# Kernel optimization log

Hardware: AMD Instinct MI355X
Metric: run time of the kernel (lower is better)

Reference implementation:

```python
import jax, jax.numpy as jnp
import numpy as np

H = 1024      # hidden_size
V = 32000     # output_size (vocab)
L = 512       # max_length (encoder positions)
B = 256       # batch


def setup_inputs() -> dict:
    key = jax.random.key(0)
    ks = jax.random.split(key, 12)
    s = 0.02
    return {
        "input": jax.random.randint(ks[0], (B,), 0, V),
        "hidden": jax.random.normal(ks[1], (1, B, H), jnp.float32),
        "encoder_outputs": jax.random.normal(ks[2], (L, H), jnp.float32),
        # learned params (PyTorch layout: Linear weight is [out, in])
        "emb": jax.random.normal(ks[3], (V, H), jnp.float32) * s,
        "attn_W": jax.random.normal(ks[4], (L, 2 * H), jnp.float32) * s,
        "attn_b": jnp.zeros((L,), jnp.float32),
        "comb_W": jax.random.normal(ks[5], (H, 2 * H), jnp.float32) * s,
        "comb_b": jnp.zeros((H,), jnp.float32),
        "W_ih": jax.random.normal(ks[6], (3 * H, H), jnp.float32) * s,
        "W_hh": jax.random.normal(ks[7], (3 * H, H), jnp.float32) * s,
        "b_ih": jnp.zeros((3 * H,), jnp.float32),
        "b_hh": jnp.zeros((3 * H,), jnp.float32),
        "out_W": jax.random.normal(ks[8], (V, H), jnp.float32) * s,
        "out_b": jnp.zeros((V,), jnp.float32),
    }


def reference(input, hidden, encoder_outputs, emb, attn_W, attn_b,
              comb_W, comb_b, W_ih, W_hh, b_ih, b_hh, out_W, out_b):
    h = hidden[0]                                   # [B,H]
    embedded = emb[input]                           # [B,H] (dropout in eval mode = identity)
    attn_logits = jnp.concatenate([embedded, h], axis=1) @ attn_W.T + attn_b
    attn_weights = jax.nn.softmax(attn_logits, axis=1)        # [B,L]
    attn_applied = attn_weights @ encoder_outputs              # [B,H]
    x = jnp.concatenate([embedded, attn_applied], axis=1) @ comb_W.T + comb_b
    x = jax.nn.relu(x)                                         # [B,H]
    # single-step GRU (PyTorch gate layout: r, z, n)
    gi = x @ W_ih.T + b_ih                                     # [B,3H]
    gh = h @ W_hh.T + b_hh                                     # [B,3H]
    gi_r, gi_z, gi_n = jnp.split(gi, 3, axis=1)
    gh_r, gh_z, gh_n = jnp.split(gh, 3, axis=1)
    r = jax.nn.sigmoid(gi_r + gh_r)
    z = jax.nn.sigmoid(gi_z + gh_z)
    n = jnp.tanh(gi_n + r * gh_n)
    h_new = (1.0 - z) * n + z * h                              # [B,H]
    output = jax.nn.log_softmax(h_new @ out_W.T + out_b, axis=1)  # [B,V]
    return output, h_new[None], attn_weights
```

## Files before the change

### kernel.cpp

```cpp
#include <hip/hip_runtime.h>
#include <hip/hip_bf16.h>
#include <cstdint>

#define DEVI __device__ __forceinline__

typedef __bf16 bf16x8 __attribute__((ext_vector_type(8)));
typedef float  f32x4  __attribute__((ext_vector_type(4)));

constexpr int Hdim = 1024;
constexpr int Vdim = 32000;
constexpr int Ldim = 512;
constexpr int Bdim = 256;

DEVI unsigned short f2bf(float f) {
  __bf16 h = (__bf16)f;
  return __builtin_bit_cast(unsigned short, h);
}

DEVI void load_lds16(const void* g, void* l) {
  __builtin_amdgcn_global_load_lds(
      (const __attribute__((address_space(1))) unsigned int*)g,
      (__attribute__((address_space(3))) unsigned int*)l, 16, 0, 0);
}

constexpr int GF_NKT = 32;

__global__ __launch_bounds__(256, 2)
void gemm_flat(const unsigned short* __restrict__ A,
               const float* __restrict__ W,
               const float* __restrict__ bias,
               float* __restrict__ C,
               float2* __restrict__ plse)
{
  __shared__ float lW[4][64 * 32];

  const int t    = threadIdx.x;
  const int lane = t & 63;
  const int wv   = t >> 6;
  const int r16  = lane & 15;
  const int k8   = (lane >> 4) * 8;
  const int s0   = (lane >> 4) * 2;
  const int n0   = blockIdx.x * 64;
  const int drow0 = wv * 16 + (lane >> 3);

  uint4 aset[4][4];
  f32x4 acc[4][4];
#pragma unroll
  for (int m = 0; m < 4; ++m)
#pragma unroll
    for (int n = 0; n < 4; ++n)
#pragma unroll
      for (int r = 0; r < 4; ++r) acc[m][n][r] = 0.f;

#define ISSUE_A(SET, KT) do {                                                  \
    const int ko_ = (KT) * 32 + k8;                                            \
    _Pragma("unroll")                                                          \
    for (int m = 0; m < 4; ++m)                                                \
      aset[SET][m] = *reinterpret_cast<const uint4*>(                          \
          A + (size_t)(wv * 64 + m * 16 + r16) * 1024 + ko_);                  \
  } while (0)

#define ISSUE_W(BUF, KT) do {                                                  \
    _Pragma("unroll")                                                          \
    for (int q = 0; q < 2; ++q) {                                              \
      const int row_ = drow0 + q * 8;                                          \
      const float* src_ = W + (size_t)(n0 + row_) * 1024 + (KT) * 32           \
                          + (((lane & 7) ^ (row_ & 7)) * 4);                   \
      load_lds16(src_, &lW[BUF][(wv * 2 + q) * 256]);                          \
    }                                                                          \
  } while (0)

#define STEP_COMPUTE(P) do {                                                   \
    bf16x8 bw[4];                                                              \
    _Pragma("unroll")                                                          \
    for (int n = 0; n < 4; ++n) {                                              \
      const int row_ = n * 16 + r16;                                           \
      const int sw_  = row_ & 7;                                               \
      f32x4 w0 = *reinterpret_cast<const f32x4*>(                              \
          &lW[P][row_ * 32 + ((s0 ^ sw_) * 4)]);                               \
      f32x4 w1 = *reinterpret_cast<const f32x4*>(                              \
          &lW[P][row_ * 32 + (((s0 + 1) ^ sw_) * 4)]);                         \
      bf16x8 v;                                                                \
      v[0] = (__bf16)w0[0]; v[1] = (__bf16)w0[1];                              \
      v[2] = (__bf16)w0[2]; v[3] = (__bf16)w0[3];                              \
      v[4] = (__bf16)w1[0]; v[5] = (__bf16)w1[1];                              \
      v[6] = (__bf16)w1[2]; v[7] = (__bf16)w1[3];                              \
      bw[n] = v;                                                               \
    }                                                                          \
    _Pragma("unroll")                                                          \
    for (int m = 0; m < 4; ++m) {                                              \
      bf16x8 am = __builtin_bit_cast(bf16x8, aset[P][m]);                      \
      _Pragma("unroll")                                                        \
      for (int n = 0; n < 4; ++n)                                              \
        acc[m][n] = __builtin_amdgcn_mfma_f32_16x16x32_bf16(am, bw[n],         \
                                                            acc[m][n], 0,0,0);\
    }                                                                          \
  } while (0)

#define STEP(P, I) do {                                                        \
    asm volatile("s_waitcnt vmcnt(12)" ::: "memory");                          \
    __builtin_amdgcn_sched_barrier(0);                                         \
    __builtin_amdgcn_s_barrier();                                              \
    __builtin_amdgcn_sched_barrier(0);                                         \
    { const int kn_ = ((I) + 3 < GF_NKT) ? (I) + 3 : GF_NKT - 1;               \
      ISSUE_A((P + 3) & 3, kn_); ISSUE_W((P + 3) & 3, kn_); }                  \
    __builtin_amdgcn_sched_barrier(0);                                         \
    STEP_COMPUTE(P);                                                           \
    __builtin_amdgcn_sched_barrier(0);                                         \
  } while (0)

  ISSUE_A(0, 0); ISSUE_W(0, 0);
  ISSUE_A(1, 1); ISSUE_W(1, 1);
  ISSUE_A(2, 2); ISSUE_W(2, 2);

  for (int ib = 0; ib < GF_NKT; ib += 4) {
    STEP(0, ib);
    STEP(1, ib + 1);
    STEP(2, ib + 2);
    STEP(3, ib + 3);
  }

#undef STEP
#undef STEP_COMPUTE
#undef ISSUE_W
#undef ISSUE_A

#pragma unroll
  for (int n = 0; n < 4; ++n) {
    const int col = n0 + n * 16 + r16;
    const float bv = bias[col];
#pragma unroll
    for (int m = 0; m < 4; ++m) {
      const int rbase = wv * 64 + m * 16 + (lane >> 4) * 4;
#pragma unroll
      for (int r = 0; r < 4; ++r) {
        const float v = acc[m][n][r] + bv;
        acc[m][n][r] = v;
        C[(size_t)(rbase + r) * Vdim + col] = v;
      }
    }
  }
#pragma unroll
  for (int m = 0; m < 4; ++m) {
#pragma unroll
    for (int r = 0; r < 4; ++r) {
      float mx = fmaxf(fmaxf(acc[m][0][r], acc[m][1][r]),
                       fmaxf(acc[m][2][r], acc[m][3][r]));
#pragma unroll
      for (int o = 1; o < 16; o <<= 1) mx = fmaxf(mx, __shfl_xor(mx, o, 16));
      float s = 0.f;
#pragma unroll
      for (int n = 0; n < 4; ++n) s += __expf(acc[m][n][r] - mx);
#pragma unroll
      for (int o = 1; o < 16; o <<= 1) s += __shfl_xor(s, o, 16);
      if (r16 == 0) {
        const int row = wv * 64 + m * 16 + (lane >> 4) * 4 + r;
        plse[(size_t)row * gridDim.x + blockIdx.x] = make_float2(mx, s);
      }
    }
  }
}

template<int WM, bool ABF16, bool DUAL>
__global__ __launch_bounds__(256, 2)
void gemm_bt(const void* __restrict__ Av0, const float* __restrict__ Wt0,
             const void* __restrict__ Av1, const float* __restrict__ Wt1,
             const float* __restrict__ bias,
             float* __restrict__ C0, float* __restrict__ C1,
             int K, int ldc, int col_off, int act, int aact0,
             int nsplit)
{
  constexpr int MT    = 4 * WM;
  constexpr int PITCH = 40;
  constexpr int ITA   = MT / 32;
  constexpr int MR    = WM / 16;

  __shared__ unsigned short lA[2 * MT * PITCH];
  __shared__ unsigned short lW[2 * 64 * PITCH];

  const int t  = threadIdx.x;
  const int m0 = blockIdx.y * MT;
  const int n0 = blockIdx.x * 64;

  int kz = blockIdx.z, half = 0;
  if (DUAL) { half = (kz >= nsplit) ? 1 : 0; kz -= half * nsplit; }
  const int NK = K / (32 * nsplit);
  const int kb = kz * NK;

  const void*  Av = (DUAL && half) ? Av1 : Av0;
  const float* Wt = (DUAL && half) ? Wt1 : Wt0;
  float*       C  = (DUAL && half) ? C1  : C0;
  const int  aact = (DUAL && half) ? 0 : aact0;

  const int tr = t >> 3;
  const int tc = (t & 7) * 4;

  const float*          Af = ABF16 ? nullptr : ((const float*)Av) + (size_t)m0 * K;
  const unsigned short* Ab = ABF16 ? ((const unsigned short*)Av) + (size_t)m0 * K : nullptr;
  const float*          Wb = Wt + (size_t)n0 * K;

  const int lane = t & 63;
  const int wv   = t >> 6;
  const int r16  = lane & 15;
  const int k8   = (lane >> 4) * 8;

  f32x4 acc[MR][4];
#pragma unroll
  for (int m = 0; m < MR; ++m)
#pragma unroll
    for (int n = 0; n < 4; ++n)
#pragma unroll
      for (int r = 0; r < 4; ++r) acc[m][n][r] = 0.f;

  struct RS { f32x4 ra[ITA]; ushort4 rab[ITA]; f32x4 rw[2]; };

  auto loadT = [&](RS& rg, int kt) {
    const int ko = (kb + kt) * 32 + tc;
    if constexpr (ABF16) {
      const unsigned short* ap = Ab + ko;
#pragma unroll
      for (int i = 0; i < ITA; ++i)
        rg.rab[i] = *reinterpret_cast<const ushort4*>(ap + (size_t)(tr + 32 * i) * K);
    } else {
      const float* ap = Af + ko;
#pragma unroll
      for (int i = 0; i < ITA; ++i)
        rg.ra[i] = *reinterpret_cast<const f32x4*>(ap + (size_t)(tr + 32 * i) * K);
    }
    const float* wp = Wb + ko;
#pragma unroll
    for (int i = 0; i < 2; ++i)
      rg.rw[i] = *reinterpret_cast<const f32x4*>(wp + (size_t)(tr + 32 * i) * K);
  };

  auto storeT = [&](RS& rg, int bo) {
    unsigned short* sA = &lA[bo * MT * PITCH];
    unsigned short* sW = &lW[bo * 64 * PITCH];
#pragma unroll
    for (int i = 0; i < ITA; ++i) {
      ushort4 u;
      if constexpr (ABF16) u = rg.rab[i];
      else {
        f32x4 v = rg.ra[i];
        if (aact) { v[0]=fmaxf(v[0],0.f); v[1]=fmaxf(v[1],0.f);
                    v[2]=fmaxf(v[2],0.f); v[3]=fmaxf(v[3],0.f); }
        u.x = f2bf(v[0]); u.y = f2bf(v[1]); u.z = f2bf(v[2]); u.w = f2bf(v[3]);
      }
      *reinterpret_cast<ushort4*>(&sA[(tr + 32 * i) * PITCH + tc]) = u;
    }
#pragma unroll
    for (int i = 0; i < 2; ++i) {
      f32x4 v = rg.rw[i]; ushort4 u;
      u.x = f2bf(v[0]); u.y = f2bf(v[1]); u.z = f2bf(v[2]); u.w = f2bf(v[3]);
      *reinterpret_cast<ushort4*>(&sW[(tr + 32 * i) * PITCH + tc]) = u;
    }
  };

  auto comp = [&](int bo) {
    const unsigned short* sA = &lA[bo * MT * PITCH];
    const unsigned short* sW = &lW[bo * 64 * PITCH];
    bf16x8 af[MR], bfr[4];
#pragma unroll
    for (int m = 0; m < MR; ++m)
      af[m] = *reinterpret_cast<const bf16x8*>(&sA[(wv * WM + m * 16 + r16) * PITCH + k8]);
#pragma unroll
    for (int n = 0; n < 4; ++n)
      bfr[n] = *reinterpret_cast<const bf16x8*>(&sW[(n * 16 + r16) * PITCH + k8]);
#pragma unroll
    for (int m = 0; m < MR; ++m)
#pragma unroll
      for (int n = 0; n < 4; ++n)
        acc[m][n] = __builtin_amdgcn_mfma_f32_16x16x32_bf16(af[m], bfr[n], acc[m][n], 0, 0, 0);
  };

#define GB_BARRIER() do { \
    asm volatile("s_waitcnt lgkmcnt(0)" ::: "memory"); \
    __builtin_amdgcn_sched_barrier(0); \
    __builtin_amdgcn_s_barrier(); \
  } while (0)

  RS ra_, rb_;
  loadT(ra_, 0);
  loadT(rb_, 1);
  storeT(ra_, 0);
  GB_BARRIER();

  for (int kt = 0; kt < NK; kt += 2) {
    if (kt + 2 < NK) loadT(ra_, kt + 2);
    comp(0);
    storeT(rb_, 1);
    GB_BARRIER();
    if (kt + 3 < NK) loadT(rb_, kt + 3);
    comp(1);
    if (kt + 2 < NK) {
      storeT(ra_, 0);
      GB_BARRIER();
    }
  }
#undef GB_BARRIER

#pragma unroll
  for (int n = 0; n < 4; ++n) {
    const int col = n0 + n * 16 + r16;
    const float bv = (bias && nsplit == 1) ? bias[col] : 0.f;
#pragma unroll
    for (int m = 0; m < MR; ++m) {
      const int rbase = m0 + wv * WM + m * 16 + (lane >> 4) * 4;
#pragma unroll
      for (int r = 0; r < 4; ++r) {
        float v = acc[m][n][r] + bv;
        if (act) v = fmaxf(v, 0.f);
        if (nsplit > 1) {
          atomicAdd(&C[(size_t)(rbase + r) * ldc + col_off + col], v);
        } else {
          C[(size_t)(rbase + r) * ldc + col_off + col] = v;
        }
      }
    }
  }
}

__global__ void prep_kernel(const int* __restrict__ ids, const float* __restrict__ hid,
                            const float* __restrict__ emb,
                            const float* __restrict__ attn_b, const float* __restrict__ comb_b,
                            const float* __restrict__ b_ih, const float* __restrict__ b_hh,
                            float* __restrict__ X0, float* __restrict__ X1,
                            float* __restrict__ alog, float* __restrict__ xact,
                            float* __restrict__ gi, float* __restrict__ gh)
{
  const int b = blockIdx.x, t = threadIdx.x;
  const int row = ids[b];
  f32x4 e = *reinterpret_cast<const f32x4*>(emb + (size_t)row * Hdim + t * 4);
  *reinterpret_cast<f32x4*>(X0 + (size_t)b * 2048 + t * 4) = e;
  *reinterpret_cast<f32x4*>(X1 + (size_t)b * 2048 + t * 4) = e;
  f32x4 h = *reinterpret_cast<const f32x4*>(hid + (size_t)b * Hdim + t * 4);
  *reinterpret_cast<f32x4*>(X0 + (size_t)b * 2048 + 1024 + t * 4) = h;
  f32x4 z4 = {0.f, 0.f, 0.f, 0.f};
  *reinterpret_cast<f32x4*>(X1 + (size_t)b * 2048 + 1024 + t * 4) = z4;
  if (t < 128)
    *reinterpret_cast<f32x4*>(alog + (size_t)b * Ldim + t * 4) =
        *reinterpret_cast<const f32x4*>(attn_b + t * 4);
  *reinterpret_cast<f32x4*>(xact + (size_t)b * Hdim + t * 4) =
      *reinterpret_cast<const f32x4*>(comb_b + t * 4);
#pragma unroll
  for (int i = 0; i < 3; ++i) {
    *reinterpret_cast<f32x4*>(gi + (size_t)b * 3072 + i * 1024 + t * 4) =
        *reinterpret_cast<const f32x4*>(b_ih + i * 1024 + t * 4);
    *reinterpret_cast<f32x4*>(gh + (size_t)b * 3072 + i * 1024 + t * 4) =
        *reinterpret_cast<const f32x4*>(b_hh + i * 1024 + t * 4);
  }
}

__global__ void transpose_kernel(const float* __restrict__ enc, float* __restrict__ encT)
{
  __shared__ float tile[64][65];
  const int l0 = blockIdx.x * 64, h0 = blockIdx.y * 64;
  const int t = threadIdx.x;
  const int c = t & 63, rr = t >> 6;
#pragma unroll
  for (int p = 0; p < 16; ++p) {
    const int r = p * 4 + rr;
    tile[r][c] = enc[(size_t)(l0 + r) * Hdim + h0 + c];
  }
  __syncthreads();
#pragma unroll
  for (int p = 0; p < 16; ++p) {
    const int r = p * 4 + rr;
    encT[(size_t)(h0 + r) * Ldim + l0 + c] = tile[c][r];
  }
}

__global__ void attn_softmax_kernel(const float* __restrict__ logits, float* __restrict__ wout)
{
  __shared__ float red[256];
  const int b = blockIdx.x, t = threadIdx.x;
  const float x0 = logits[b * Ldim + t];
  const float x1 = logits[b * Ldim + 256 + t];
  red[t] = fmaxf(x0, x1); __syncthreads();
  for (int o = 128; o > 0; o >>= 1) { if (t < o) red[t] = fmaxf(red[t], red[t + o]); __syncthreads(); }
  const float m = red[0]; __syncthreads();
  const float e0 = __expf(x0 - m), e1 = __expf(x1 - m);
  red[t] = e0 + e1; __syncthreads();
  for (int o = 128; o > 0; o >>= 1) { if (t < o) red[t] += red[t + o]; __syncthreads(); }
  const float inv = 1.f / red[0];
  wout[b * Ldim + t]       = e0 * inv;
  wout[b * Ldim + 256 + t] = e1 * inv;
}

DEVI float sigm(float x) { return 1.f / (1.f + __expf(-x)); }

__global__ void gru_kernel(const float* __restrict__ gi, const float* __restrict__ gh,
                           const float* __restrict__ hin,
                           float* __restrict__ hnew, unsigned short* __restrict__ hnbf)
{
  const int idx = blockIdx.x * 256 + threadIdx.x;
  const int b = idx >> 10, j = idx & 1023;
  const float* gib = gi + (size_t)b * 3072;
  const float* ghb = gh + (size_t)b * 3072;
  const float r = sigm(gib[j] + ghb[j]);
  const float z = sigm(gib[1024 + j] + ghb[1024 + j]);
  const float n = tanhf(gib[2048 + j] + r * ghb[2048 + j]);
  const float h = hin[idx];
  const float hn = (1.f - z) * n + z * h;
  hnew[idx] = hn;
  hnbf[idx] = f2bf(hn);
}

__global__ void lse_reduce(const float2* __restrict__ part, int npart,
                           float* __restrict__ lse)
{
  __shared__ float rm[256], rs[256];
  const int b = blockIdx.x, t = threadIdx.x;
  float m = -1e30f, s = 0.f;
  for (int j = t; j < npart; j += 256) {
    const float2 p = part[(size_t)b * npart + j];
    const float nm = fmaxf(m, p.x);
    s = s * __expf(m - nm) + p.y * __expf(p.x - nm);
    m = nm;
  }
  rm[t] = m; rs[t] = s; __syncthreads();
  for (int o = 128; o > 0; o >>= 1) {
    if (t < o) {
      const float m2 = rm[t + o], s2 = rs[t + o];
      const float nm = fmaxf(rm[t], m2);
      rs[t] = rs[t] * __expf(rm[t] - nm) + s2 * __expf(m2 - nm);
      rm[t] = nm;
    }
    __syncthreads();
  }
  if (t == 0) lse[b] = rm[0] + __logf(rs[0]);
}

__global__ void lsm_sub(const float* __restrict__ lse, float* __restrict__ out)
{
  const int b = blockIdx.x >> 3, c = blockIdx.x & 7;
  const float l = lse[b];
  f32x4* row4 = reinterpret_cast<f32x4*>(out + (size_t)b * Vdim) + c * 1000;
  for (int i = threadIdx.x; i < 1000; i += 256) {
    f32x4 x = row4[i];
    x[0] -= l; x[1] -= l; x[2] -= l; x[3] -= l;
    row4[i] = x;
  }
}

extern "C" void kernel_launch(void* const* d_in, const int* in_sizes, int n_in,
                              void* d_out, int out_size, void* d_ws, size_t ws_size,
                              hipStream_t stream)
{
  (void)in_sizes; (void)n_in; (void)out_size; (void)ws_size;

  const int*   ids    = (const int*)  d_in[0];
  const float* hid    = (const float*)d_in[1];
  const float* enc    = (const float*)d_in[2];
  const float* emb    = (const float*)d_in[3];
  const float* attn_W = (const float*)d_in[4];
  const float* attn_b = (const float*)d_in[5];
  const float* comb_W = (const float*)d_in[6];
  const float* comb_b = (const float*)d_in[7];
  const float* W_ih   = (const float*)d_in[8];
  const float* W_hh   = (const float*)d_in[9];
  const float* b_ih   = (const float*)d_in[10];
  const float* b_hh   = (const float*)d_in[11];
  const float* out_W  = (const float*)d_in[12];
  const float* out_b  = (const float*)d_in[13];

  float* out_logits = (float*)d_out;
  float* out_h      = out_logits + (size_t)Bdim * Vdim;
  float* out_attw   = out_h + (size_t)Bdim * Hdim;

  char* w = (char*)d_ws;
  float* X0   = (float*)w; w += (size_t)Bdim * 2048 * 4;
  float* X1   = (float*)w; w += (size_t)Bdim * 2048 * 4;
  float* encT = (float*)w; w += (size_t)Hdim * Ldim * 4;
  float* alog = (float*)w; w += (size_t)Bdim * Ldim * 4;
  float* xact = (float*)w; w += (size_t)Bdim * Hdim * 4;
  float* gi   = (float*)w; w += (size_t)Bdim * 3 * Hdim * 4;
  float* gh   = (float*)w; w += (size_t)Bdim * 3 * Hdim * 4;
  unsigned short* hnbf = (unsigned short*)w; w += (size_t)Bdim * Hdim * 2;
  float2* plse = (float2*)w; w += (size_t)Bdim * (Vdim / 64) * 8;
  float* lse  = (float*)w; w += (size_t)Bdim * 4;

  prep_kernel<<<Bdim, 256, 0, stream>>>(ids, hid, emb, attn_b, comb_b, b_ih, b_hh,
                                        X0, X1, alog, xact, gi, gh);
  transpose_kernel<<<dim3(Ldim / 64, Hdim / 64), 256, 0, stream>>>(enc, encT);

  gemm_bt<32, false, false><<<dim3(Ldim / 64, 2, 8), 256, 0, stream>>>(
      X0, attn_W, nullptr, nullptr, nullptr, alog, nullptr,
      2048, Ldim, 0, 0, 0, 8);
  attn_softmax_kernel<<<Bdim, 256, 0, stream>>>(alog, out_attw);

  gemm_bt<32, false, false><<<dim3(Hdim / 64, 2, 4), 256, 0, stream>>>(
      out_attw, encT, nullptr, nullptr, nullptr, X1, nullptr,
      512, 2048, 1024, 0, 0, 4);

  gemm_bt<32, false, false><<<dim3(Hdim / 64, 2, 8), 256, 0, stream>>>(
      X1, comb_W, nullptr, nullptr, nullptr, xact, nullptr,
      2048, Hdim, 0, 0, 0, 8);

  gemm_bt<32, false, true><<<dim3(3 * Hdim / 64, 2, 8), 256, 0, stream>>>(
      xact, W_ih, hid, W_hh, nullptr, gi, gh,
      1024, 3 * Hdim, 0, 0, 1, 4);

  gru_kernel<<<Bdim * Hdim / 256, 256, 0, stream>>>(gi, gh, hid, out_h, hnbf);

  gemm_flat<<<Vdim / 64, 256, 0, stream>>>(hnbf, out_W, out_b, out_logits, plse);

  lse_reduce<<<Bdim, 256, 0, stream>>>(plse, Vdim / 64, lse);
  lsm_sub<<<Bdim * 8, 256, 0, stream>>>(lse, out_logits);
}
```

Measured before the change: 138.0 us.

## Stage full-K bf16 weight tile in LDS for output projection GEMM

Replaces the pipelined output-projection GEMM with a variant where each block handles 32 vocab columns, converts the whole 32x1024 weight slice to bf16 once into swizzled LDS, and then streams A with simple double-buffered register prefetch. This drops the per-step fp32-to-bf16 conversion, the LDS round trips of fp32 weights and the per-step barriers. In exchange it doubles the grid and the partial logsumexp entries, uses 64KB of LDS per block, which limits occupancy, and reloads A from global memory for every block.

```diff
diff --git a/kernel.cpp b/kernel.cpp
--- a/kernel.cpp
+++ b/kernel.cpp
@@ -17,116 +17,87 @@
   return __builtin_bit_cast(unsigned short, h);
 }
 
-DEVI void load_lds16(const void* g, void* l) {
-  __builtin_amdgcn_global_load_lds(
-      (const __attribute__((address_space(1))) unsigned int*)g,
-      (__attribute__((address_space(3))) unsigned int*)l, 16, 0, 0);
-}
-
-constexpr int GF_NKT = 32;
-
 __global__ __launch_bounds__(256, 2)
-void gemm_flat(const unsigned short* __restrict__ A,
-               const float* __restrict__ W,
-               const float* __restrict__ bias,
-               float* __restrict__ C,
-               float2* __restrict__ plse)
-{
-  __shared__ float lW[4][64 * 32];
+void gemm_flat2(const unsigned short* __restrict__ A,
+                const float* __restrict__ W,
+                const float* __restrict__ bias,
+                float* __restrict__ C,
+                float2* __restrict__ plse)
+{
+  __shared__ unsigned short lW[32 * 1024];
 
   const int t    = threadIdx.x;
   const int lane = t & 63;
   const int wv   = t >> 6;
   const int r16  = lane & 15;
   const int k8   = (lane >> 4) * 8;
-  const int s0   = (lane >> 4) * 2;
-  const int n0   = blockIdx.x * 64;
-  const int drow0 = wv * 16 + (lane >> 3);
-
-  uint4 aset[4][4];
-  f32x4 acc[4][4];
+  const int n0   = blockIdx.x * 32;
+
+  f32x4 acc[4][2];
 #pragma unroll
   for (int m = 0; m < 4; ++m)
 #pragma unroll
-    for (int n = 0; n < 4; ++n)
+    for (int n = 0; n < 2; ++n)
 #pragma unroll
       for (int r = 0; r < 4; ++r) acc[m][n][r] = 0.f;
 
-#define ISSUE_A(SET, KT) do {                                                  \
+#pragma unroll 2
+  for (int r = 0; r < 8; ++r) {
+    const int row = wv * 8 + r;
+    const float* src = W + (size_t)(n0 + row) * 1024;
+    f32x4 v[4];
+#pragma unroll
+    for (int j = 0; j < 4; ++j)
+      v[j] = *reinterpret_cast<const f32x4*>(src + j * 256 + lane * 4);
+#pragma unroll
+    for (int j = 0; j < 4; ++j) {
+      ushort4 u;
+      u.x = f2bf(v[j][0]); u.y = f2bf(v[j][1]);
+      u.z = f2bf(v[j][2]); u.w = f2bf(v[j][3]);
+      const int byte = row * 2048 + (j * 64 + lane) * 8;
+      *reinterpret_cast<ushort4*>((char*)lW + (byte ^ ((row & 7) << 4))) = u;
+    }
+  }
+
+  uint4 apf0[4], apf1[4];
+
+#define LOADA(ARR, KT) do {                                                    \
     const int ko_ = (KT) * 32 + k8;                                            \
     _Pragma("unroll")                                                          \
     for (int m = 0; m < 4; ++m)                                                \
-      aset[SET][m] = *reinterpret_cast<const uint4*>(                          \
+      ARR[m] = *reinterpret_cast<const uint4*>(                                \
           A + (size_t)(wv * 64 + m * 16 + r16) * 1024 + ko_);                  \
   } while (0)
 
-#define ISSUE_W(BUF, KT) do {                                                  \
+#define COMP(ARR, KT) do {                                                     \
     _Pragma("unroll")                                                          \
-    for (int q = 0; q < 2; ++q) {                                              \
-      const int row_ = drow0 + q * 8;                                          \
-      const float* src_ = W + (size_t)(n0 + row_) * 1024 + (KT) * 32           \
-                          + (((lane & 7) ^ (row_ & 7)) * 4);                   \
-      load_lds16(src_, &lW[BUF][(wv * 2 + q) * 256]);                          \
+    for (int n = 0; n < 2; ++n) {                                              \
+      const int nr_  = n * 16 + r16;                                           \
+      const int rby_ = nr_ * 2048 + (KT) * 64 + (lane >> 4) * 16;              \
+      bf16x8 bw = *reinterpret_cast<const bf16x8*>(                            \
+          (const char*)lW + (rby_ ^ ((nr_ & 7) << 4)));                        \
+      _Pragma("unroll")                                                        \
+      for (int m = 0; m < 4; ++m)                                              \
+        acc[m][n] = __builtin_amdgcn_mfma_f32_16x16x32_bf16(                   \
+            __builtin_bit_cast(bf16x8, ARR[m]), bw, acc[m][n], 0, 0, 0);       \
     }                                                                          \
   } while (0)
 
-#define STEP_COMPUTE(P) do {                                                   \
-    bf16x8 bw[4];                                                              \
-    _Pragma("unroll")                                                          \
-    for (int n = 0; n < 4; ++n) {                                              \
-      const int row_ = n * 16 + r16;                                           \
-      const int sw_  = row_ & 7;                                               \
-      f32x4 w0 = *reinterpret_cast<const f32x4*>(                              \
-          &lW[P][row_ * 32 + ((s0 ^ sw_) * 4)]);                               \
-      f32x4 w1 = *reinterpret_cast<const f32x4*>(                              \
-          &lW[P][row_ * 32 + (((s0 + 1) ^ sw_) * 4)]);                         \
-      bf16x8 v;                                                                \
-      v[0] = (__bf16)w0[0]; v[1] = (__bf16)w0[1];                              \
-      v[2] = (__bf16)w0[2]; v[3] = (__bf16)w0[3];                              \
-      v[4] = (__bf16)w1[0]; v[5] = (__bf16)w1[1];                              \
-      v[6] = (__bf16)w1[2]; v[7] = (__bf16)w1[3];                              \
-      bw[n] = v;                                                               \
-    }                                                                          \
-    _Pragma("unroll")                                                          \
-    for (int m = 0; m < 4; ++m) {                                              \
-      bf16x8 am = __builtin_bit_cast(bf16x8, aset[P][m]);                      \
-      _Pragma("unroll")                                                        \
-      for (int n = 0; n < 4; ++n)                                              \
-        acc[m][n] = __builtin_amdgcn_mfma_f32_16x16x32_bf16(am, bw[n],         \
-                                                            acc[m][n], 0,0,0);\
-    }                                                                          \
-  } while (0)
-
-#define STEP(P, I) do {                                                        \
-    asm volatile("s_waitcnt vmcnt(12)" ::: "memory");                          \
-    __builtin_amdgcn_sched_barrier(0);                                         \
-    __builtin_amdgcn_s_barrier();                                              \
-    __builtin_amdgcn_sched_barrier(0);                                         \
-    { const int kn_ = ((I) + 3 < GF_NKT) ? (I) + 3 : GF_NKT - 1;               \
-      ISSUE_A((P + 3) & 3, kn_); ISSUE_W((P + 3) & 3, kn_); }                  \
-    __builtin_amdgcn_sched_barrier(0);                                         \
-    STEP_COMPUTE(P);                                                           \
-    __builtin_amdgcn_sched_barrier(0);                                         \
-  } while (0)
-
-  ISSUE_A(0, 0); ISSUE_W(0, 0);
-  ISSUE_A(1, 1); ISSUE_W(1, 1);
-  ISSUE_A(2, 2); ISSUE_W(2, 2);
-
-  for (int ib = 0; ib < GF_NKT; ib += 4) {
-    STEP(0, ib);
-    STEP(1, ib + 1);
-    STEP(2, ib + 2);
-    STEP(3, ib + 3);
-  }
-
-#undef STEP
-#undef STEP_COMPUTE
-#undef ISSUE_W
-#undef ISSUE_A
-
-#pragma unroll
-  for (int n = 0; n < 4; ++n) {
+  LOADA(apf0, 0);
+  __syncthreads();
+
+  for (int kt = 0; kt < 32; kt += 2) {
+    LOADA(apf1, kt + 1);
+    COMP(apf0, kt);
+    LOADA(apf0, (kt + 2 < 32) ? kt + 2 : 31);
+    COMP(apf1, kt + 1);
+  }
+
+#undef COMP
+#undef LOADA
+
+#pragma unroll
+  for (int n = 0; n < 2; ++n) {
     const int col = n0 + n * 16 + r16;
     const float bv = bias[col];
 #pragma unroll
@@ -144,13 +115,10 @@
   for (int m = 0; m < 4; ++m) {
 #pragma unroll
     for (int r = 0; r < 4; ++r) {
-      float mx = fmaxf(fmaxf(acc[m][0][r], acc[m][1][r]),
-                       fmaxf(acc[m][2][r], acc[m][3][r]));
+      float mx = fmaxf(acc[m][0][r], acc[m][1][r]);
 #pragma unroll
       for (int o = 1; o < 16; o <<= 1) mx = fmaxf(mx, __shfl_xor(mx, o, 16));
-      float s = 0.f;
-#pragma unroll
-      for (int n = 0; n < 4; ++n) s += __expf(acc[m][n][r] - mx);
+      float s = __expf(acc[m][0][r] - mx) + __expf(acc[m][1][r] - mx);
 #pragma unroll
       for (int o = 1; o < 16; o <<= 1) s += __shfl_xor(s, o, 16);
       if (r16 == 0) {
@@ -477,7 +445,7 @@
   float* gi   = (float*)w; w += (size_t)Bdim * 3 * Hdim * 4;
   float* gh   = (float*)w; w += (size_t)Bdim * 3 * Hdim * 4;
   unsigned short* hnbf = (unsigned short*)w; w += (size_t)Bdim * Hdim * 2;
-  float2* plse = (float2*)w; w += (size_t)Bdim * (Vdim / 64) * 8;
+  float2* plse = (float2*)w; w += (size_t)Bdim * (Vdim / 32) * 8;
   float* lse  = (float*)w; w += (size_t)Bdim * 4;
 
   prep_kernel<<<Bdim, 256, 0, stream>>>(ids, hid, emb, attn_b, comb_b, b_ih, b_hh,
@@ -503,8 +471,8 @@
 
   gru_kernel<<<Bdim * Hdim / 256, 256, 0, stream>>>(gi, gh, hid, out_h, hnbf);
 
-  gemm_flat<<<Vdim / 64, 256, 0, stream>>>(hnbf, out_W, out_b, out_logits, plse);
-
-  lse_reduce<<<Bdim, 256, 0, stream>>>(plse, Vdim / 64, lse);
+  gemm_flat2<<<Vdim / 32, 256, 0, stream>>>(hnbf, out_W, out_b, out_logits, plse);
+
+  lse_reduce<<<Bdim, 256, 0, stream>>>(plse, Vdim / 32, lse);
   lsm_sub<<<Bdim * 8, 256, 0, stream>>>(lse, out_logits);
 }
```

Measured after the change: 176.7 us. +28.1%, slower.
